# Kernel tuning notes

Hardware: AMD Instinct MI355X
Metric: run time of the kernel (lower is better)

Reference implementation:

```python
import jax, jax.numpy as jnp
import numpy as np

VISION_TOKEN_TYPE = 1
B, L, D, FF = 2, 2048, 1024, 4096


def setup_inputs() -> dict:
    key = jax.random.key(0)
    ks = jax.random.split(key, 8)
    s_in = 1.0 / np.sqrt(D)
    s_ff = 1.0 / np.sqrt(FF)
    return {
        "hidden_states": jax.random.normal(ks[0], (B, L, D), dtype=jnp.float32),
        "token_type_ids": jax.random.randint(ks[1], (B, L), 0, 2, dtype=jnp.int64),
        "v_gate": jax.random.normal(ks[2], (FF, D), dtype=jnp.float32) * s_in,
        "v_up": jax.random.normal(ks[3], (FF, D), dtype=jnp.float32) * s_in,
        "v_down": jax.random.normal(ks[4], (D, FF), dtype=jnp.float32) * s_ff,
        "l_gate": jax.random.normal(ks[5], (FF, D), dtype=jnp.float32) * s_in,
        "l_up": jax.random.normal(ks[6], (FF, D), dtype=jnp.float32) * s_in,
        "l_down": jax.random.normal(ks[7], (D, FF), dtype=jnp.float32) * s_ff,
    }


def _swiglu_mlp(x, w_gate, w_up, w_down):
    # x: (B, L, D); torch Linear stores weight as (out, in) -> contract on last dim
    g = jax.nn.silu(jnp.einsum("bld,fd->blf", x, w_gate))
    u = jnp.einsum("bld,fd->blf", x, w_up)
    return jnp.einsum("blf,df->bld", g * u, w_down)


def _vision_mask(token_type_ids):
    # vision token iff this token AND the next token are vision type; last col False
    t = token_type_ids == VISION_TOKEN_TYPE
    inner = t[:, :-1] & t[:, 1:]
    return jnp.concatenate([inner, jnp.zeros((t.shape[0], 1), dtype=bool)], axis=1)


def reference(hidden_states, token_type_ids, v_gate, v_up, v_down, l_gate, l_up, l_down):
    vision_mask = _vision_mask(token_type_ids)  # (B, L) bool
    vis_out = _swiglu_mlp(hidden_states, v_gate, v_up, v_down)
    lang_out = _swiglu_mlp(hidden_states, l_gate, l_up, l_down)
    return jnp.where(vision_mask[:, :, None], vis_out, lang_out)
```

## Files before the change

kernel.cpp:

```cpp
#include <hip/hip_runtime.h>
#include <hip/hip_bf16.h>
#include <stdint.h>


#define TOKENS 4096
#define SEQ    2048
#define DIM    1024
#define FFDIM  4096
#define MAXPAD 4608

typedef __attribute__((ext_vector_type(8))) short bf16x8;
typedef __attribute__((ext_vector_type(4))) float f32x4;

#define GAS __attribute__((address_space(1)))
#define LAS __attribute__((address_space(3)))

__device__ inline unsigned short f2bf(float x) {
    union { float f; unsigned int u; } c; c.f = x;
    unsigned int r = c.u + 0x7FFFu + ((c.u >> 16) & 1u);
    return (unsigned short)(r >> 16);
}
__device__ inline float bf2f(unsigned short u) {
    union { unsigned int i; float f; } c; c.i = ((unsigned int)u) << 16;
    return c.f;
}

struct __align__(16) us8 { unsigned short v[8]; };

__global__ __launch_bounds__(1024) void scan_kernel(const int* __restrict__ tt,
                                                    int* __restrict__ src_of,
                                                    int* __restrict__ counts) {
    __shared__ int wsum[16];
    const int tid  = threadIdx.x;
    const int lane = tid & 63;
    const int wav  = tid >> 6;

    for (int i = tid; i < MAXPAD; i += 1024) src_of[i] = -1;

    const int t0 = tid * 4;
    int v[4], cnt = 0;
#pragma unroll
    for (int j = 0; j < 4; ++j) {
        const int t = t0 + j;
        const int l = t & (SEQ - 1);
        int vis = 0;
        if (l < SEQ - 1) vis = (tt[t] == 1) & (tt[t + 1] == 1);
        v[j] = vis; cnt += vis;
    }

    int s = cnt;
#pragma unroll
    for (int off = 1; off < 64; off <<= 1) {
        const int o = __shfl_up(s, off, 64);
        if (lane >= off) s += o;
    }
    if (lane == 63) wsum[wav] = s;
    __syncthreads();
    if (wav == 0 && lane < 16) {
        int w = wsum[lane];
#pragma unroll
        for (int off = 1; off < 16; off <<= 1) {
            const int o = __shfl_up(w, off, 16);
            if (lane >= off) w += o;
        }
        wsum[lane] = w;
    }
    __syncthreads();

    const int wbase  = wav ? wsum[wav - 1] : 0;
    const int incl   = wbase + s;
    const int excl   = incl - cnt;
    const int totalV = wsum[15];
    const int padNv  = (totalV + 127) & ~127;
    int pv = excl;
    int pl = padNv + (t0 - excl);
#pragma unroll
    for (int j = 0; j < 4; ++j) {
        const int t = t0 + j;
        if (v[j]) src_of[pv++] = t; else src_of[pl++] = t;
    }
    if (tid == 0) {
        const int Nl = TOKENS - totalV;
        counts[0] = padNv;
        counts[1] = padNv + ((Nl + 127) & ~127);
    }
}

__device__ inline void gather_body(const float* __restrict__ hs, const int* __restrict__ src_of,
                                   unsigned short* __restrict__ Xg, int gid) {
    const int row = gid >> 7;
    const int c   = (gid & 127) * 8;
    const int src = src_of[row];
    us8 o;
    if (src >= 0) {
        const float4 a = *reinterpret_cast<const float4*>(hs + (size_t)src * DIM + c);
        const float4 b = *reinterpret_cast<const float4*>(hs + (size_t)src * DIM + c + 4);
        o.v[0] = f2bf(a.x); o.v[1] = f2bf(a.y); o.v[2] = f2bf(a.z); o.v[3] = f2bf(a.w);
        o.v[4] = f2bf(b.x); o.v[5] = f2bf(b.y); o.v[6] = f2bf(b.z); o.v[7] = f2bf(b.w);
    } else {
#pragma unroll
        for (int j = 0; j < 8; ++j) o.v[j] = 0;
    }
    *reinterpret_cast<us8*>(Xg + (size_t)row * DIM + c) = o;
}

__global__ void gather_cast(const float* __restrict__ hs, const int* __restrict__ src_of,
                            unsigned short* __restrict__ Xg) {
    gather_body(hs, src_of, Xg, blockIdx.x * 256 + threadIdx.x);
}

__device__ inline void cast8(const float* __restrict__ in, unsigned short* __restrict__ out, int i) {
    const float4 a = *reinterpret_cast<const float4*>(in + i);
    const float4 b = *reinterpret_cast<const float4*>(in + i + 4);
    us8 o;
    o.v[0] = f2bf(a.x); o.v[1] = f2bf(a.y); o.v[2] = f2bf(a.z); o.v[3] = f2bf(a.w);
    o.v[4] = f2bf(b.x); o.v[5] = f2bf(b.y); o.v[6] = f2bf(b.z); o.v[7] = f2bf(b.w);
    *reinterpret_cast<us8*>(out + i) = o;
}

__global__ void prep_kernel(const float* __restrict__ hs, const int* __restrict__ src_of,
                            unsigned short* __restrict__ Xg,
                            const float* __restrict__ s0, const float* __restrict__ s1,
                            const float* __restrict__ s2, const float* __restrict__ s3,
                            const float* __restrict__ s4, const float* __restrict__ s5,
                            unsigned short* __restrict__ d0, unsigned short* __restrict__ d1,
                            unsigned short* __restrict__ d2, unsigned short* __restrict__ d3,
                            unsigned short* __restrict__ d4, unsigned short* __restrict__ d5) {
    const int m = blockIdx.y;
    if (m == 0) {
        gather_body(hs, src_of, Xg, blockIdx.x * 256 + threadIdx.x);
    } else {
        const int i = (blockIdx.x * 256 + threadIdx.x) * 8;
        if (i >= FFDIM * DIM) return;
        const float* s = (m == 1) ? s0 : (m == 2) ? s1 : (m == 3) ? s2 : (m == 4) ? s3 : (m == 5) ? s4 : s5;
        unsigned short* d = (m == 1) ? d0 : (m == 2) ? d1 : (m == 3) ? d2 : (m == 4) ? d3 : (m == 5) ? d4 : d5;
        cast8(s, d, i);
    }
}

__global__ void cast4_kernel(const float* __restrict__ s0, const float* __restrict__ s1,
                             const float* __restrict__ s2, const float* __restrict__ s3,
                             unsigned short* __restrict__ d0, unsigned short* __restrict__ d1,
                             unsigned short* __restrict__ d2, unsigned short* __restrict__ d3) {
    const int i = (blockIdx.x * 256 + threadIdx.x) * 8;
    const int m = blockIdx.y;
    const float* s = (m == 0) ? s0 : (m == 1) ? s1 : (m == 2) ? s2 : s3;
    unsigned short* d = (m == 0) ? d0 : (m == 1) ? d1 : (m == 2) ? d2 : d3;
    cast8(s, d, i);
}

__global__ void cast2_kernel(const float* __restrict__ s0, const float* __restrict__ s1,
                             unsigned short* __restrict__ d0, unsigned short* __restrict__ d1) {
    const int i = (blockIdx.x * 256 + threadIdx.x) * 8;
    const float* s = blockIdx.y ? s1 : s0;
    unsigned short* d = blockIdx.y ? d1 : d0;
    cast8(s, d, i);
}

__global__ __launch_bounds__(256, 4) void gemm_p1(
    const unsigned short* __restrict__ A,
    const unsigned short* __restrict__ B0_v, const unsigned short* __restrict__ B1_v,
    const unsigned short* __restrict__ B0_l, const unsigned short* __restrict__ B1_l,
    unsigned short* __restrict__ H,
    const int* __restrict__ counts)
{
    __shared__ unsigned short Ls[256 * 64];

    const int m0 = blockIdx.y * 128;
    const int padNv = counts[0], padTot = counts[1];
    if (m0 >= padTot) return;
    const int expert = (m0 >= padNv);
    const unsigned short* B0 = expert ? B0_l : B0_v;
    const unsigned short* B1 = expert ? B1_l : B1_v;

    const int tid  = threadIdx.x;
    const int wid  = tid >> 6;
    const int lane = tid & 63;
    const int n0   = blockIdx.x * 64;

    constexpr int NI = 8;
    const unsigned short* src[NI];
    int loff[NI];
    const int cs = ((lane & 7) ^ (lane >> 3)) * 8;
#pragma unroll
    for (int i = 0; i < NI; ++i) {
        const int g = wid * 64 + i * 8 + (lane >> 3);
        const unsigned short* p;
        if (g < 128) {
            p = A + (size_t)(m0 + g) * DIM;
        } else {
            const int br = g - 128;
            p = (br < 64) ? (B0 + (size_t)(n0 + br) * DIM) : (B1 + (size_t)(n0 + br - 64) * DIM);
        }
        src[i] = p + cs;
        loff[i] = (wid * 64 + i * 8) * 64;
    }

    const int rlo = lane & 15;
    const int sw7 = rlo & 7;

    f32x4 acc[2][8];
#pragma unroll
    for (int i = 0; i < 2; ++i)
#pragma unroll
        for (int j = 0; j < 8; ++j)
            acc[i][j] = (f32x4){0.f, 0.f, 0.f, 0.f};

    const int NKT = DIM / 64;
#pragma unroll 1
    for (int kt = 0; kt < NKT; ++kt) {
        if (kt) __syncthreads();
        const int c = kt * 64;
#pragma unroll
        for (int i = 0; i < NI; ++i)
            __builtin_amdgcn_global_load_lds((const GAS void*)(src[i] + c),
                                             (LAS void*)&Ls[loff[i]], 16, 0, 0);
        asm volatile("s_waitcnt vmcnt(0)" ::: "memory");
        __syncthreads();

#pragma unroll
        for (int kh = 0; kh < 2; ++kh) {
            const int kc    = (lane >> 4) + kh * 4;
            const int swoff = (kc ^ sw7) * 8;
            const bf16x8 af0 = *reinterpret_cast<const bf16x8*>(&Ls[(wid * 32 + rlo) * 64 + swoff]);
            const bf16x8 af1 = *reinterpret_cast<const bf16x8*>(&Ls[(wid * 32 + 16 + rlo) * 64 + swoff]);
#pragma unroll
            for (int n = 0; n < 8; ++n) {
                const bf16x8 bfr = *reinterpret_cast<const bf16x8*>(&Ls[(128 + n * 16 + rlo) * 64 + swoff]);
                acc[0][n] = __builtin_amdgcn_mfma_f32_16x16x32_bf16(af0, bfr, acc[0][n], 0, 0, 0);
                acc[1][n] = __builtin_amdgcn_mfma_f32_16x16x32_bf16(af1, bfr, acc[1][n], 0, 0, 0);
            }
        }
    }

    const int rbase = m0 + wid * 32 + ((lane >> 4) * 4);
    const int cin   = lane & 15;
#pragma unroll
    for (int fr = 0; fr < 2; ++fr)
#pragma unroll
        for (int reg = 0; reg < 4; ++reg) {
            const int row = rbase + fr * 16 + reg;
#pragma unroll
            for (int n = 0; n < 4; ++n) {
                const float g = acc[fr][n][reg];
                const float u = acc[fr][n + 4][reg];
                const float h = g / (1.0f + __expf(-g)) * u;
                H[(size_t)row * FFDIM + n0 + n * 16 + cin] = f2bf(h);
            }
        }
}

__global__ __launch_bounds__(256, 4) void gemm_p2(
    const unsigned short* __restrict__ A,
    const unsigned short* __restrict__ Bd_v, const unsigned short* __restrict__ Bd_l,
    unsigned short* __restrict__ P,
    const int* __restrict__ counts)
{
    __shared__ unsigned short Ls[256 * 64];

    const int m0 = blockIdx.y * 128;
    const int padNv = counts[0], padTot = counts[1];
    if (m0 >= padTot) return;
    const unsigned short* B0 = (m0 >= padNv) ? Bd_l : Bd_v;

    const int tid  = threadIdx.x;
    const int wid  = tid >> 6;
    const int lane = tid & 63;
    const int wr   = wid >> 1;
    const int wc   = wid & 1;
    const int n0   = blockIdx.x * 128;
    const int kbase = blockIdx.z * (FFDIM / 2);

    constexpr int NI = 8;
    const unsigned short* src[NI];
    int loff[NI];
    const int cs = ((lane & 7) ^ (lane >> 3)) * 8;
#pragma unroll
    for (int i = 0; i < NI; ++i) {
        const int g = wid * 64 + i * 8 + (lane >> 3);
        const unsigned short* p = (g < 128)
            ? A + (size_t)(m0 + g) * FFDIM
            : B0 + (size_t)(n0 + g - 128) * FFDIM;
        src[i] = p + kbase + cs;
        loff[i] = (wid * 64 + i * 8) * 64;
    }

    const int rlo = lane & 15;
    const int sw7 = rlo & 7;

    f32x4 acc[4][4];
#pragma unroll
    for (int i = 0; i < 4; ++i)
#pragma unroll
        for (int j = 0; j < 4; ++j)
            acc[i][j] = (f32x4){0.f, 0.f, 0.f, 0.f};

    const int NKT = (FFDIM / 2) / 64;
    bf16x8 af[4], bf[4];
#pragma unroll 1
    for (int kt = 0; kt < NKT; ++kt) {
        if (kt) __syncthreads();
        const int c = kt * 64;
#pragma unroll
        for (int i = 0; i < NI; ++i)
            __builtin_amdgcn_global_load_lds((const GAS void*)(src[i] + c),
                                             (LAS void*)&Ls[loff[i]], 16, 0, 0);
        asm volatile("s_waitcnt vmcnt(0)" ::: "memory");
        __syncthreads();

#pragma unroll
        for (int kh = 0; kh < 2; ++kh) {
            const int kc    = (lane >> 4) + kh * 4;
            const int swoff = (kc ^ sw7) * 8;
#pragma unroll
            for (int i = 0; i < 4; ++i)
                af[i] = *reinterpret_cast<const bf16x8*>(&Ls[(wr * 64 + i * 16 + rlo) * 64 + swoff]);
#pragma unroll
            for (int j = 0; j < 4; ++j)
                bf[j] = *reinterpret_cast<const bf16x8*>(&Ls[(128 + wc * 64 + j * 16 + rlo) * 64 + swoff]);

#pragma unroll
            for (int i = 0; i < 4; ++i)
#pragma unroll
                for (int j = 0; j < 4; ++j)
                    acc[i][j] = __builtin_amdgcn_mfma_f32_16x16x32_bf16(af[i], bf[j], acc[i][j], 0, 0, 0);
        }
    }

    unsigned short* Pz = P + (size_t)blockIdx.z * MAXPAD * DIM;
    const int rbase = m0 + wr * 64 + ((lane >> 4) * 4);
    const int cin   = lane & 15;
#pragma unroll
    for (int i = 0; i < 4; ++i)
#pragma unroll
        for (int reg = 0; reg < 4; ++reg) {
            const int row = rbase + i * 16 + reg;
#pragma unroll
            for (int j = 0; j < 4; ++j)
                Pz[(size_t)row * DIM + n0 + wc * 64 + j * 16 + cin] = f2bf(acc[i][j][reg]);
        }
}

__global__ void reduce_kernel(const unsigned short* __restrict__ P,
                              const int* __restrict__ src_of,
                              float* __restrict__ O) {
    const int gid = blockIdx.x * 256 + threadIdx.x;
    const int row = gid >> 7;
    const int c   = (gid & 127) * 8;
    const int src = src_of[row];
    if (src < 0) return;
    const us8 a = *reinterpret_cast<const us8*>(P + (size_t)row * DIM + c);
    const us8 b = *reinterpret_cast<const us8*>(P + (size_t)(MAXPAD + row) * DIM + c);
    float4 o0, o1;
    o0.x = bf2f(a.v[0]) + bf2f(b.v[0]);
    o0.y = bf2f(a.v[1]) + bf2f(b.v[1]);
    o0.z = bf2f(a.v[2]) + bf2f(b.v[2]);
    o0.w = bf2f(a.v[3]) + bf2f(b.v[3]);
    o1.x = bf2f(a.v[4]) + bf2f(b.v[4]);
    o1.y = bf2f(a.v[5]) + bf2f(b.v[5]);
    o1.z = bf2f(a.v[6]) + bf2f(b.v[6]);
    o1.w = bf2f(a.v[7]) + bf2f(b.v[7]);
    float* dst = O + (size_t)src * DIM + c;
    *reinterpret_cast<float4*>(dst)     = o0;
    *reinterpret_cast<float4*>(dst + 4) = o1;
}

extern "C" void kernel_launch(void* const* d_in, const int* in_sizes, int n_in,
                              void* d_out, int out_size, void* d_ws, size_t ws_size,
                              hipStream_t stream) {
    const float* hs = (const float*)d_in[0];
    const int*   tt = (const int*)d_in[1];
    const float* w_vg = (const float*)d_in[2];
    const float* w_vu = (const float*)d_in[3];
    const float* w_vd = (const float*)d_in[4];
    const float* w_lg = (const float*)d_in[5];
    const float* w_lu = (const float*)d_in[6];
    const float* w_ld = (const float*)d_in[7];
    float* out = (float*)d_out;
    char* ws = (char*)d_ws;

    const size_t MATB = (size_t)FFDIM * DIM * 2;
    const size_t XGB  = (size_t)MAXPAD * DIM * 2;
    const size_t HSZ  = (size_t)MAXPAD * FFDIM * 2;

    int* counts = (int*)ws;
    int* src_of = (int*)(ws + 64);
    unsigned short* Xg = (unsigned short*)(ws + 32768);

    const int NELEM = FFDIM * DIM;
    const size_t need_big = 32768 + XGB + 6 * MATB + HSZ;

    scan_kernel<<<1, 1024, 0, stream>>>(tt, src_of, counts);

    if (ws_size >= need_big) {
        unsigned short* Wg_v = (unsigned short*)(ws + 32768 + XGB);
        unsigned short* Wu_v = (unsigned short*)(ws + 32768 + XGB + MATB);
        unsigned short* Wg_l = (unsigned short*)(ws + 32768 + XGB + MATB * 2);
        unsigned short* Wu_l = (unsigned short*)(ws + 32768 + XGB + MATB * 3);
        unsigned short* Wd_v = (unsigned short*)(ws + 32768 + XGB + MATB * 4);
        unsigned short* Wd_l = (unsigned short*)(ws + 32768 + XGB + MATB * 5);
        unsigned short* H    = (unsigned short*)(ws + 32768 + XGB + MATB * 6);
        unsigned short* Part = Wg_v;

        dim3 gp(MAXPAD * 128 / 256, 7);
        prep_kernel<<<gp, 256, 0, stream>>>(hs, src_of, Xg,
                                            w_vg, w_vu, w_lg, w_lu, w_vd, w_ld,
                                            Wg_v, Wu_v, Wg_l, Wu_l, Wd_v, Wd_l);

        dim3 g1(FFDIM / 64, MAXPAD / 128);
        gemm_p1<<<g1, 256, 0, stream>>>(Xg, Wg_v, Wu_v, Wg_l, Wu_l, H, counts);

        dim3 g2(DIM / 128, MAXPAD / 128, 2);
        gemm_p2<<<g2, 256, 0, stream>>>(H, Wd_v, Wd_l, Part, counts);

        reduce_kernel<<<MAXPAD * 128 / 256, 256, 0, stream>>>(Part, src_of, out);
    } else {
        unsigned short* Wg_v = (unsigned short*)(ws + 32768 + XGB);
        unsigned short* Wu_v = (unsigned short*)(ws + 32768 + XGB + MATB);
        unsigned short* Wg_l = (unsigned short*)(ws + 32768 + XGB + MATB * 2);
        unsigned short* Wu_l = (unsigned short*)(ws + 32768 + XGB + MATB * 3);
        unsigned short* H    = (unsigned short*)(ws + 32768 + XGB + MATB * 4);
        unsigned short* Wd_v = (unsigned short*)(ws + 32768);
        unsigned short* Wd_l = (unsigned short*)(ws + 32768 + MATB);
        unsigned short* Part = (unsigned short*)(ws + 32768 + MATB * 2);

        gather_cast<<<MAXPAD * 128 / 256, 256, 0, stream>>>(hs, src_of, Xg);

        dim3 gc4(NELEM / 2048, 4);
        cast4_kernel<<<gc4, 256, 0, stream>>>(w_vg, w_vu, w_lg, w_lu, Wg_v, Wu_v, Wg_l, Wu_l);

        dim3 g1(FFDIM / 64, MAXPAD / 128);
        gemm_p1<<<g1, 256, 0, stream>>>(Xg, Wg_v, Wu_v, Wg_l, Wu_l, H, counts);

        dim3 gc2(NELEM / 2048, 2);
        cast2_kernel<<<gc2, 256, 0, stream>>>(w_vd, w_ld, Wd_v, Wd_l);

        dim3 g2(DIM / 128, MAXPAD / 128, 2);
        gemm_p2<<<g2, 256, 0, stream>>>(H, Wd_v, Wd_l, Part, counts);

        reduce_kernel<<<MAXPAD * 128 / 256, 256, 0, stream>>>(Part, src_of, out);
    }
}
```

Before: 177.2 us.

## Drop split-K in down-projection GEMM and scatter fp32 output directly

The down-projection GEMM no longer splits K across two blocks writing bf16 partials. Each block now computes a 128x64 tile over the full K range and scatters fp32 results straight to the output rows via src_of, so the separate reduce kernel goes away. This removes the partial-buffer write and reread, a kernel launch, and the bf16 rounding of the partials. In exchange each block has a smaller N tile with a longer K loop and lower MFMA reuse per LDS load. The total block count stays the same.

```diff
diff --git a/kernel.cpp b/kernel.cpp
--- a/kernel.cpp
+++ b/kernel.cpp
@@ -253,10 +253,11 @@
 __global__ __launch_bounds__(256, 4) void gemm_p2(
     const unsigned short* __restrict__ A,
     const unsigned short* __restrict__ Bd_v, const unsigned short* __restrict__ Bd_l,
-    unsigned short* __restrict__ P,
+    const int* __restrict__ src_of,
+    float* __restrict__ O,
     const int* __restrict__ counts)
 {
-    __shared__ unsigned short Ls[256 * 64];
+    __shared__ unsigned short Ls[192 * 64];
 
     const int m0 = blockIdx.y * 128;
     const int padNv = counts[0], padTot = counts[1];
@@ -266,37 +267,33 @@
     const int tid  = threadIdx.x;
     const int wid  = tid >> 6;
     const int lane = tid & 63;
-    const int wr   = wid >> 1;
-    const int wc   = wid & 1;
-    const int n0   = blockIdx.x * 128;
-    const int kbase = blockIdx.z * (FFDIM / 2);
-
-    constexpr int NI = 8;
+    const int n0   = blockIdx.x * 64;
+
+    constexpr int NI = 6;
     const unsigned short* src[NI];
     int loff[NI];
     const int cs = ((lane & 7) ^ (lane >> 3)) * 8;
 #pragma unroll
     for (int i = 0; i < NI; ++i) {
-        const int g = wid * 64 + i * 8 + (lane >> 3);
+        const int g = wid * 48 + i * 8 + (lane >> 3);
         const unsigned short* p = (g < 128)
             ? A + (size_t)(m0 + g) * FFDIM
             : B0 + (size_t)(n0 + g - 128) * FFDIM;
-        src[i] = p + kbase + cs;
-        loff[i] = (wid * 64 + i * 8) * 64;
+        src[i] = p + cs;
+        loff[i] = (wid * 48 + i * 8) * 64;
     }
 
     const int rlo = lane & 15;
     const int sw7 = rlo & 7;
 
-    f32x4 acc[4][4];
-#pragma unroll
-    for (int i = 0; i < 4; ++i)
+    f32x4 acc[2][4];
+#pragma unroll
+    for (int i = 0; i < 2; ++i)
 #pragma unroll
         for (int j = 0; j < 4; ++j)
             acc[i][j] = (f32x4){0.f, 0.f, 0.f, 0.f};
 
-    const int NKT = (FFDIM / 2) / 64;
-    bf16x8 af[4], bf[4];
+    const int NKT = FFDIM / 64;
 #pragma unroll 1
     for (int kt = 0; kt < NKT; ++kt) {
         if (kt) __syncthreads();
@@ -312,57 +309,32 @@
         for (int kh = 0; kh < 2; ++kh) {
             const int kc    = (lane >> 4) + kh * 4;
             const int swoff = (kc ^ sw7) * 8;
-#pragma unroll
-            for (int i = 0; i < 4; ++i)
-                af[i] = *reinterpret_cast<const bf16x8*>(&Ls[(wr * 64 + i * 16 + rlo) * 64 + swoff]);
-#pragma unroll
-            for (int j = 0; j < 4; ++j)
-                bf[j] = *reinterpret_cast<const bf16x8*>(&Ls[(128 + wc * 64 + j * 16 + rlo) * 64 + swoff]);
-
-#pragma unroll
-            for (int i = 0; i < 4; ++i)
-#pragma unroll
-                for (int j = 0; j < 4; ++j)
-                    acc[i][j] = __builtin_amdgcn_mfma_f32_16x16x32_bf16(af[i], bf[j], acc[i][j], 0, 0, 0);
-        }
-    }
-
-    unsigned short* Pz = P + (size_t)blockIdx.z * MAXPAD * DIM;
-    const int rbase = m0 + wr * 64 + ((lane >> 4) * 4);
+            const bf16x8 af0 = *reinterpret_cast<const bf16x8*>(&Ls[(wid * 32 + rlo) * 64 + swoff]);
+            const bf16x8 af1 = *reinterpret_cast<const bf16x8*>(&Ls[(wid * 32 + 16 + rlo) * 64 + swoff]);
+#pragma unroll
+            for (int n = 0; n < 4; ++n) {
+                const bf16x8 bfr = *reinterpret_cast<const bf16x8*>(&Ls[(128 + n * 16 + rlo) * 64 + swoff]);
+                acc[0][n] = __builtin_amdgcn_mfma_f32_16x16x32_bf16(af0, bfr, acc[0][n], 0, 0, 0);
+                acc[1][n] = __builtin_amdgcn_mfma_f32_16x16x32_bf16(af1, bfr, acc[1][n], 0, 0, 0);
+            }
+        }
+    }
+
+    const int rbase = m0 + wid * 32 + ((lane >> 4) * 4);
     const int cin   = lane & 15;
 #pragma unroll
-    for (int i = 0; i < 4; ++i)
+    for (int fr = 0; fr < 2; ++fr)
 #pragma unroll
         for (int reg = 0; reg < 4; ++reg) {
-            const int row = rbase + i * 16 + reg;
-#pragma unroll
-            for (int j = 0; j < 4; ++j)
-                Pz[(size_t)row * DIM + n0 + wc * 64 + j * 16 + cin] = f2bf(acc[i][j][reg]);
-        }
-}
-
-__global__ void reduce_kernel(const unsigned short* __restrict__ P,
-                              const int* __restrict__ src_of,
-                              float* __restrict__ O) {
-    const int gid = blockIdx.x * 256 + threadIdx.x;
-    const int row = gid >> 7;
-    const int c   = (gid & 127) * 8;
-    const int src = src_of[row];
-    if (src < 0) return;
-    const us8 a = *reinterpret_cast<const us8*>(P + (size_t)row * DIM + c);
-    const us8 b = *reinterpret_cast<const us8*>(P + (size_t)(MAXPAD + row) * DIM + c);
-    float4 o0, o1;
-    o0.x = bf2f(a.v[0]) + bf2f(b.v[0]);
-    o0.y = bf2f(a.v[1]) + bf2f(b.v[1]);
-    o0.z = bf2f(a.v[2]) + bf2f(b.v[2]);
-    o0.w = bf2f(a.v[3]) + bf2f(b.v[3]);
-    o1.x = bf2f(a.v[4]) + bf2f(b.v[4]);
-    o1.y = bf2f(a.v[5]) + bf2f(b.v[5]);
-    o1.z = bf2f(a.v[6]) + bf2f(b.v[6]);
-    o1.w = bf2f(a.v[7]) + bf2f(b.v[7]);
-    float* dst = O + (size_t)src * DIM + c;
-    *reinterpret_cast<float4*>(dst)     = o0;
-    *reinterpret_cast<float4*>(dst + 4) = o1;
+            const int row = rbase + fr * 16 + reg;
+            const int s   = src_of[row];
+            if (s >= 0) {
+                float* dst = O + (size_t)s * DIM + n0;
+#pragma unroll
+                for (int n = 0; n < 4; ++n)
+                    dst[n * 16 + cin] = acc[fr][n][reg];
+            }
+        }
 }
 
 extern "C" void kernel_launch(void* const* d_in, const int* in_sizes, int n_in,
@@ -400,7 +372,6 @@
         unsigned short* Wd_v = (unsigned short*)(ws + 32768 + XGB + MATB * 4);
         unsigned short* Wd_l = (unsigned short*)(ws + 32768 + XGB + MATB * 5);
         unsigned short* H    = (unsigned short*)(ws + 32768 + XGB + MATB * 6);
-        unsigned short* Part = Wg_v;
 
         dim3 gp(MAXPAD * 128 / 256, 7);
         prep_kernel<<<gp, 256, 0, stream>>>(hs, src_of, Xg,
@@ -410,10 +381,8 @@
         dim3 g1(FFDIM / 64, MAXPAD / 128);
         gemm_p1<<<g1, 256, 0, stream>>>(Xg, Wg_v, Wu_v, Wg_l, Wu_l, H, counts);
 
-        dim3 g2(DIM / 128, MAXPAD / 128, 2);
-        gemm_p2<<<g2, 256, 0, stream>>>(H, Wd_v, Wd_l, Part, counts);
-
-        reduce_kernel<<<MAXPAD * 128 / 256, 256, 0, stream>>>(Part, src_of, out);
+        dim3 g2(DIM / 64, MAXPAD / 128);
+        gemm_p2<<<g2, 256, 0, stream>>>(H, Wd_v, Wd_l, src_of, out, counts);
     } else {
         unsigned short* Wg_v = (unsigned short*)(ws + 32768 + XGB);
         unsigned short* Wu_v = (unsigned short*)(ws + 32768 + XGB + MATB);
@@ -422,7 +391,6 @@
         unsigned short* H    = (unsigned short*)(ws + 32768 + XGB + MATB * 4);
         unsigned short* Wd_v = (unsigned short*)(ws + 32768);
         unsigned short* Wd_l = (unsigned short*)(ws + 32768 + MATB);
-        unsigned short* Part = (unsigned short*)(ws + 32768 + MATB * 2);
 
         gather_cast<<<MAXPAD * 128 / 256, 256, 0, stream>>>(hs, src_of, Xg);
 
@@ -435,9 +403,7 @@
         dim3 gc2(NELEM / 2048, 2);
         cast2_kernel<<<gc2, 256, 0, stream>>>(w_vd, w_ld, Wd_v, Wd_l);
 
-        dim3 g2(DIM / 128, MAXPAD / 128, 2);
-        gemm_p2<<<g2, 256, 0, stream>>>(H, Wd_v, Wd_l, Part, counts);
-
-        reduce_kernel<<<MAXPAD * 128 / 256, 256, 0, stream>>>(Part, src_of, out);
-    }
-}
+        dim3 g2(DIM / 64, MAXPAD / 128);
+        gemm_p2<<<g2, 256, 0, stream>>>(H, Wd_v, Wd_l, src_of, out, counts);
+    }
+}
```

Result: no change. 177.2 us (+0.0%).
